# Performance work log

Hardware: AMD Instinct MI355X
Metric: run time of the kernel (lower is better)

Reference implementation:

```python
import jax, jax.numpy as jnp
import numpy as np

_EPS = 1e-6
_ZCA_EPS = 1e-5
NEG_SLOPE_ATTN = 0.2   # LeakyReLU inside score_mlp
NEG_SLOPE_FFN = 0.1    # VNLinearLeakyReLU negative_slope


def _safe_norm(x, axis, keepdims=False):
    # norm with zero-gradient at exactly-zero vectors (matches torch subgradient)
    sq = jnp.sum(x * x, axis=axis, keepdims=keepdims)
    safe = jnp.where(sq == 0, 1.0, sq)
    return jnp.sqrt(safe) * (sq > 0)


def vn_linear(W, x):
    # W: (out, in); x: (B, C_in, 3, N) -> (B, C_out, 3, N)
    return jnp.einsum('oi,bivn->bovn', W, x)


def zca_layernorm(x, gamma):
    # x: (B, C, 3, N); whiten the 3D vector components per batch element
    B, C = x.shape[0], x.shape[1]
    xf = x.reshape(B, C, 3, -1).transpose(0, 2, 1, 3).reshape(B, 3, -1)
    xf = xf.astype(jnp.float32)
    mu = xf.mean(axis=-1, keepdims=True)
    xc = xf - mu
    M = xc.shape[-1]
    cov = (xc @ xc.transpose(0, 2, 1)) / (float(M) + _EPS)  # (B,3,3)
    cov = cov + _ZCA_EPS * jnp.eye(3, dtype=cov.dtype)[None]
    w, V = jnp.linalg.eigh(cov)
    w = jnp.maximum(w, _ZCA_EPS)
    Wm = (V * jax.lax.rsqrt(w)[:, None, :]) @ V.transpose(0, 2, 1)  # (B,3,3)
    xw = Wm @ xc
    xw = xw.reshape(B, 3, C, -1).transpose(0, 2, 1, 3).reshape(x.shape).astype(x.dtype)
    return xw * gamma[None, :, None, None]


def cwsa_attention(x, pos, Wq, Wk, Wv, Wo, W1, b1, W2, b2):
    q = vn_linear(Wq, x)  # (B,C,3,N)
    k = vn_linear(Wk, x)
    v = vn_linear(Wv, x)
    qk = q.transpose(0, 3, 1, 2)  # (B,N,C,3)
    kk = k.transpose(0, 3, 1, 2)
    vv = v.transpose(0, 3, 1, 2)
    rel = qk[:, :, None, :, :] - kk[:, None, :, :, :]      # (B,N,N,C,3)
    rel_norm = _safe_norm(rel, axis=-1)                    # (B,N,N,C)
    rel_mean = rel_norm.mean(axis=-1, keepdims=True)       # (B,N,N,1)
    rel_pos = pos[:, :, None, :] - pos[:, None, :, :]      # (B,N,N,3)
    rel_pos_norm = _safe_norm(rel_pos, axis=-1, keepdims=True)  # (B,N,N,1)
    score_in = jnp.concatenate([rel_mean, rel_pos_norm], axis=-1)  # (B,N,N,2)
    h = jax.nn.leaky_relu(score_in @ W1.T + b1, NEG_SLOPE_ATTN)
    scores = h @ W2.T + b2                                  # (B,N,N,C)
    attn = jax.nn.softmax(scores, axis=2)                   # softmax over keys j
    out = jnp.einsum('bijk,bjkd->bikd', attn, vv)           # (B,N,C,3)
    out = out.transpose(0, 2, 3, 1)                         # (B,C,3,N)
    return vn_linear(Wo, out)


def vn_leaky_relu(p, d, ns):
    # p, d: (B, C, 3, N)
    dot = jnp.sum(p * d, axis=2, keepdims=True)
    dsq = jnp.sum(d * d, axis=2, keepdims=True)
    mask = (dot >= 0).astype(p.dtype)
    proj = p - (dot / (dsq + _EPS)) * d
    return ns * p + (1.0 - ns) * (mask * p + (1.0 - mask) * proj)


def ffn(x, Wfeat, Wdir, Wffn2):
    p = vn_linear(Wfeat, x)
    d = vn_linear(Wdir, x)
    h = vn_leaky_relu(p, d, NEG_SLOPE_FFN)
    return vn_linear(Wffn2, h)


def setup_inputs() -> dict:
    key = jax.random.key(0)
    ks = jax.random.split(key, 16)
    B, C, N = 2, 128, 256
    hidden, ratio = 64, 2
    sC = 1.0 / np.sqrt(C)
    inp = {
        'x': jax.random.normal(ks[0], (B, C, 3, N), dtype=jnp.float32),
        'pos': jax.random.normal(ks[1], (B, N, 3), dtype=jnp.float32),
        'Wq': jax.random.normal(ks[2], (C, C), dtype=jnp.float32) * sC,
        'Wk': jax.random.normal(ks[3], (C, C), dtype=jnp.float32) * sC,
        'Wv': jax.random.normal(ks[4], (C, C), dtype=jnp.float32) * sC,
        'Wo': jax.random.normal(ks[5], (C, C), dtype=jnp.float32) * sC,
        'W1': jax.random.normal(ks[6], (hidden, 2), dtype=jnp.float32) * (1.0 / np.sqrt(2.0)),
        'b1': jnp.zeros((hidden,), dtype=jnp.float32),
        'W2': jax.random.normal(ks[7], (C, hidden), dtype=jnp.float32) * (1.0 / np.sqrt(hidden)),
        'b2': jnp.zeros((C,), dtype=jnp.float32),
        'gamma1': jnp.ones((C,), dtype=jnp.float32),
        'Wfeat': jax.random.normal(ks[8], (C * ratio, C), dtype=jnp.float32) * sC,
        'Wdir': jax.random.normal(ks[9], (C * ratio, C), dtype=jnp.float32) * sC,
        'Wffn2': jax.random.normal(ks[10], (C, C * ratio), dtype=jnp.float32) * (1.0 / np.sqrt(C * ratio)),
        'gamma2': jnp.ones((C,), dtype=jnp.float32),
    }
    return inp


def reference(x, pos, Wq, Wk, Wv, Wo, W1, b1, W2, b2, gamma1, Wfeat, Wdir, Wffn2, gamma2):
    a = cwsa_attention(x, pos, Wq, Wk, Wv, Wo, W1, b1, W2, b2)
    x1 = zca_layernorm(x + a, gamma1)
    f = ffn(x1, Wfeat, Wdir, Wffn2)
    return zca_layernorm(x1 + f, gamma2)
```

## Files before the change

kernel.cpp:

```cpp
#include <hip/hip_runtime.h>
#include <math.h>

#define BB 2
#define CC 128
#define NN 256
#define HH 64
#define CHX 256
#define COLS 768
#define NEG_ATTN 0.2f
#define NEG_FFN 0.1f

typedef __attribute__((ext_vector_type(8))) short short8b;
typedef __attribute__((ext_vector_type(4))) float f32x4;

__device__ __forceinline__ unsigned bf16rne(float x) {
  unsigned u = __float_as_uint(x);
  return (u + 0x7fffu + ((u >> 16) & 1u)) >> 16;
}

__global__ __launch_bounds__(256) void k_qkv(
    const float* __restrict__ x, const float* __restrict__ Wq,
    const float* __restrict__ Wk, const float* __restrict__ Wv,
    float* __restrict__ q_t, float* __restrict__ k_nat, float* __restrict__ v_t)
{
  const int ct = blockIdx.x, which = blockIdx.y, b = blockIdx.z;
  const int col0 = ct * 16;
  __shared__ float xt[CC][16];
  const float* xb = x + (size_t)b * CC * COLS;
  for (int idx = threadIdx.x; idx < CC * 16; idx += 256) {
    int r = idx >> 4, cc = idx & 15;
    xt[r][cc] = xb[r * COLS + col0 + cc];
  }
  __syncthreads();
  const float* W = (which == 0) ? Wq : ((which == 1) ? Wk : Wv);
  const int co = threadIdx.x >> 1;
  const int cc0 = (threadIdx.x & 1) * 8;
  float acc[8];
#pragma unroll
  for (int k = 0; k < 8; k++) acc[k] = 0.f;
  const float* wrow = W + co * CC;
  for (int ci = 0; ci < CC; ci++) {
    float wv = wrow[ci];
#pragma unroll
    for (int k = 0; k < 8; k++) acc[k] = fmaf(wv, xt[ci][cc0 + k], acc[k]);
  }
#pragma unroll
  for (int k = 0; k < 8; k++) {
    int col = col0 + cc0 + k;
    int v = col >> 8, n = col & 255;
    float val = acc[k];
    if (which == 0)      q_t[((size_t)(b * NN + n) * CC + co) * 3 + v] = val;
    else if (which == 1) k_nat[(size_t)(b * CC + co) * COLS + col] = val;
    else                 v_t[((size_t)(b * NN + n) * 3 + v) * CC + co] = val;
  }
}

__global__ __launch_bounds__(256) void k_rel(
    const float* __restrict__ q_t, const float* __restrict__ k_nat,
    const float* __restrict__ pos, float* __restrict__ rm_all,
    float* __restrict__ rp_all)
{
  const int i0 = blockIdx.x * 2, b = blockIdx.y;
  const int t = threadIdx.x;
  __shared__ float qv[2 * CC * 3];
  for (int idx = t; idx < 2 * CC * 3; idx += 256)
    qv[idx] = q_t[(size_t)(b * NN + i0) * CC * 3 + idx];
  __syncthreads();
  const int j = t;
  const float* kb = k_nat + (size_t)b * CC * COLS;
  float a00 = 0.f, a01 = 0.f, a10 = 0.f, a11 = 0.f;
  for (int c = 0; c < CC; c += 2) {
    float kx0 = kb[c * COLS + j], ky0 = kb[c * COLS + 256 + j], kz0 = kb[c * COLS + 512 + j];
    float kx1 = kb[(c + 1) * COLS + j], ky1 = kb[(c + 1) * COLS + 256 + j], kz1 = kb[(c + 1) * COLS + 512 + j];
    {
      float dx = kx0 - qv[c * 3], dy = ky0 - qv[c * 3 + 1], dz = kz0 - qv[c * 3 + 2];
      float sq = dx * dx + dy * dy + dz * dz;
      a00 += (sq > 0.f) ? sqrtf(sq) : 0.f;
      dx = kx1 - qv[(c + 1) * 3]; dy = ky1 - qv[(c + 1) * 3 + 1]; dz = kz1 - qv[(c + 1) * 3 + 2];
      sq = dx * dx + dy * dy + dz * dz;
      a01 += (sq > 0.f) ? sqrtf(sq) : 0.f;
    }
    {
      const float* q1 = qv + CC * 3;
      float dx = kx0 - q1[c * 3], dy = ky0 - q1[c * 3 + 1], dz = kz0 - q1[c * 3 + 2];
      float sq = dx * dx + dy * dy + dz * dz;
      a10 += (sq > 0.f) ? sqrtf(sq) : 0.f;
      dx = kx1 - q1[(c + 1) * 3]; dy = ky1 - q1[(c + 1) * 3 + 1]; dz = kz1 - q1[(c + 1) * 3 + 2];
      sq = dx * dx + dy * dy + dz * dz;
      a11 += (sq > 0.f) ? sqrtf(sq) : 0.f;
    }
  }
  rm_all[(size_t)(b * NN + i0) * NN + j]     = (a00 + a01) * (1.f / 128.f);
  rm_all[(size_t)(b * NN + i0 + 1) * NN + j] = (a10 + a11) * (1.f / 128.f);
  float pjx = pos[(b * NN + j) * 3], pjy = pos[(b * NN + j) * 3 + 1], pjz = pos[(b * NN + j) * 3 + 2];
#pragma unroll
  for (int ii = 0; ii < 2; ii++) {
    float dx = pos[(b * NN + i0 + ii) * 3] - pjx;
    float dy = pos[(b * NN + i0 + ii) * 3 + 1] - pjy;
    float dz = pos[(b * NN + i0 + ii) * 3 + 2] - pjz;
    float sq = dx * dx + dy * dy + dz * dz;
    rp_all[(size_t)(b * NN + i0 + ii) * NN + j] = (sq > 0.f) ? sqrtf(sq) : 0.f;
  }
}

__global__ __launch_bounds__(256, 4) void k_attn(
    const float* __restrict__ rm_all, const float* __restrict__ rp_all,
    const float* __restrict__ v_t, const float* __restrict__ W1,
    const float* __restrict__ b1, const float* __restrict__ W2,
    float* __restrict__ a_nat)
{
  const int i = blockIdx.x, chalf = blockIdx.y, b = blockIdx.z;
  const int t = threadIdx.x;
  __shared__ __align__(16) short hh_s[64 * 64];
  __shared__ __align__(16) short w2_s[64 * 64];
  __shared__ float sc_s[64 * 65];
  __shared__ float rm_s[NN], rp_s[NN];

  rm_s[t] = rm_all[(size_t)(b * NN + i) * NN + t];
  rp_s[t] = rp_all[(size_t)(b * NN + i) * NN + t];
  {
    const int cl = t >> 2, h0 = (t & 3) * 16;
    const float* wrow = W2 + (size_t)(chalf * 64 + cl) * HH + h0;
#pragma unroll
    for (int e = 0; e < 8; e++) {
      unsigned lo = bf16rne(wrow[2 * e]);
      unsigned hi = bf16rne(wrow[2 * e + 1]);
      int didx = (cl * 32 + (h0 >> 1) + e) ^ ((cl & 7) << 2);
      ((unsigned*)w2_s)[didx] = lo | (hi << 16);
    }
  }
  const int h2 = (t & 31) * 2, jgrp = t >> 5;
  const float4 w1v = *reinterpret_cast<const float4*>(W1 + 2 * h2);
  const float c0 = b1[h2], c1 = b1[h2 + 1];
  __syncthreads();

  auto phase2 = [&](int q) {
#pragma unroll
    for (int jj = 0; jj < 8; jj++) {
      int jl = jgrp * 8 + jj;
      int jg = q * 64 + jl;
      float rmv = rm_s[jg], rpv = rp_s[jg];
      float g0 = fmaf(w1v.x, rmv, fmaf(w1v.y, rpv, c0));
      float g1 = fmaf(w1v.z, rmv, fmaf(w1v.w, rpv, c1));
      g0 = (g0 >= 0.f) ? g0 : NEG_ATTN * g0;
      g1 = (g1 >= 0.f) ? g1 : NEG_ATTN * g1;
      int didx = (jl * 32 + (h2 >> 1)) ^ ((jl & 7) << 2);
      ((unsigned*)hh_s)[didx] = bf16rne(g0) | (bf16rne(g1) << 16);
    }
  };

  phase2(0);
  __syncthreads();

  const int lane = t & 63, wv = t >> 6;
  const int g8 = (lane >> 4) * 8;
  const int cdx = wv * 16 + (lane & 15);
  const short8b bfr0 = *reinterpret_cast<const short8b*>(&w2_s[(cdx * 64 + g8) ^ ((cdx & 7) << 3)]);
  const short8b bfr1 = *reinterpret_cast<const short8b*>(&w2_s[(cdx * 64 + 32 + g8) ^ ((cdx & 7) << 3)]);

  const int cl = lane;
  const int par = wv;
  const int vc = chalf * 64 + cl;
  float m = -1e30f, l = 0.f, a0 = 0.f, a1 = 0.f, a2 = 0.f;

  for (int q = 0; q < 4; q++) {
#pragma unroll
    for (int jt = 0; jt < 4; jt++) {
      int jr = jt * 16 + (lane & 15);
      short8b af0 = *reinterpret_cast<const short8b*>(&hh_s[(jr * 64 + g8) ^ ((jr & 7) << 3)]);
      short8b af1 = *reinterpret_cast<const short8b*>(&hh_s[(jr * 64 + 32 + g8) ^ ((jr & 7) << 3)]);
      f32x4 acc = {0.f, 0.f, 0.f, 0.f};
      acc = __builtin_amdgcn_mfma_f32_16x16x32_bf16(af0, bfr0, acc, 0, 0, 0);
      acc = __builtin_amdgcn_mfma_f32_16x16x32_bf16(af1, bfr1, acc, 0, 0, 0);
      int row0 = jt * 16 + (lane >> 4) * 4;
      int ccol = wv * 16 + (lane & 15);
#pragma unroll
      for (int r = 0; r < 4; r++) sc_s[(row0 + r) * 65 + ccol] = acc[r];
    }
    __syncthreads();
#pragma unroll
    for (int jj = 0; jj < 16; jj++) {
      int jl = jj * 4 + par;
      int jg = q * 64 + jl;
      float s = sc_s[jl * 65 + cl];
      const float* vb = v_t + ((size_t)(b * NN + jg) * 3) * CC + vc;
      float v0 = vb[0], v1 = vb[CC], v2 = vb[2 * CC];
      float mn = fmaxf(m, s);
      float p = __expf(s - mn);
      float corr = __expf(m - mn);
      l = fmaf(l, corr, p);
      a0 = fmaf(a0, corr, p * v0);
      a1 = fmaf(a1, corr, p * v1);
      a2 = fmaf(a2, corr, p * v2);
      m = mn;
    }
    if (q < 3) phase2(q + 1);
    __syncthreads();
  }

  float* mrg = sc_s;
  if (par != 0) {
    float* mp = mrg + (cl * 3 + (par - 1)) * 5;
    mp[0] = m; mp[1] = l; mp[2] = a0; mp[3] = a1; mp[4] = a2;
  }
  __syncthreads();
  if (par == 0) {
    float M = m, L = l, A0 = a0, A1 = a1, A2 = a2;
    for (int q = 0; q < 3; q++) {
      const float* mp = mrg + (cl * 3 + q) * 5;
      float m2 = mp[0], l2 = mp[1];
      float mn = fmaxf(M, m2);
      float e1 = __expf(M - mn), e2 = __expf(m2 - mn);
      L = L * e1 + l2 * e2;
      A0 = A0 * e1 + mp[2] * e2;
      A1 = A1 * e1 + mp[3] * e2;
      A2 = A2 * e1 + mp[4] * e2;
      M = mn;
    }
    float inv = 1.f / L;
    float* ap = a_nat + (size_t)(b * CC + vc) * COLS + i;
    ap[0] = A0 * inv; ap[256] = A1 * inv; ap[512] = A2 * inv;
  }
}

__global__ __launch_bounds__(256) void k_wo_res(
    const float* __restrict__ a_nat, const float* __restrict__ Wo,
    const float* __restrict__ x, float* __restrict__ y1)
{
  const int ct = blockIdx.x, cohalf = blockIdx.y, b = blockIdx.z;
  const int col0 = ct * 16;
  __shared__ float at[CC][16];
  const float* ab = a_nat + (size_t)b * CC * COLS;
  for (int idx = threadIdx.x; idx < CC * 16; idx += 256) {
    int r = idx >> 4, cc = idx & 15;
    at[r][cc] = ab[r * COLS + col0 + cc];
  }
  __syncthreads();
  const int co = cohalf * 64 + (threadIdx.x >> 2);
  const int cc0 = (threadIdx.x & 3) * 4;
  float acc[4];
#pragma unroll
  for (int k = 0; k < 4; k++) acc[k] = 0.f;
  const float* wrow = Wo + co * CC;
  for (int ci = 0; ci < CC; ci++) {
    float wv = wrow[ci];
#pragma unroll
    for (int k = 0; k < 4; k++) acc[k] = fmaf(wv, at[ci][cc0 + k], acc[k]);
  }
  const size_t base = (size_t)(b * CC + co) * COLS + col0 + cc0;
#pragma unroll
  for (int k = 0; k < 4; k++) y1[base + k] = x[base + k] + acc[k];
}

__global__ __launch_bounds__(256) void k_stats1(
    const float* __restrict__ y, float* __restrict__ partials)
{
  const int blk = blockIdx.x, b = blockIdx.y;
  const float* yb = y + (size_t)b * CC * COLS;
  float v9[9];
#pragma unroll
  for (int k = 0; k < 9; k++) v9[k] = 0.f;
#pragma unroll
  for (int e = 0; e < 4; e++) {
    int idx = blk * 1024 + e * 256 + threadIdx.x;
    int cidx = idx >> 8, n = idx & 255;
    const float* row = yb + cidx * COLS + n;
    float v0 = row[0], v1 = row[256], v2 = row[512];
    v9[0] += v0; v9[1] += v1; v9[2] += v2;
    v9[3] += v0 * v0; v9[4] += v0 * v1; v9[5] += v0 * v2;
    v9[6] += v1 * v1; v9[7] += v1 * v2; v9[8] += v2 * v2;
  }
#pragma unroll
  for (int off = 32; off >= 1; off >>= 1)
#pragma unroll
    for (int k = 0; k < 9; k++) v9[k] += __shfl_down(v9[k], off);
  __shared__ float red[4][9];
  const int wid = threadIdx.x >> 6, lane = threadIdx.x & 63;
  if (lane == 0)
#pragma unroll
    for (int k = 0; k < 9; k++) red[wid][k] = v9[k];
  __syncthreads();
  if (threadIdx.x == 0) {
#pragma unroll
    for (int k = 0; k < 9; k++)
      partials[(size_t)(b * 32 + blk) * 9 + k] =
          ((red[0][k] + red[1][k]) + (red[2][k] + red[3][k]));
  }
}

__global__ __launch_bounds__(64) void k_zca_fin(
    const float* __restrict__ partials, float* __restrict__ stats)
{
  const int b = blockIdx.x;
  if (threadIdx.x != 0) return;
  float tot[9];
#pragma unroll
  for (int k = 0; k < 9; k++) tot[k] = 0.f;
  for (int p = 0; p < 32; p++)
#pragma unroll
    for (int k = 0; k < 9; k++) tot[k] += partials[(size_t)(b * 32 + p) * 9 + k];
  const float M = (float)(CC * NN);
  float mu0 = tot[0] / M, mu1 = tot[1] / M, mu2 = tot[2] / M;
  float A[3][3];
  A[0][0] = (tot[3] - M * mu0 * mu0) / M + 1e-5f;
  A[0][1] = A[1][0] = (tot[4] - M * mu0 * mu1) / M;
  A[0][2] = A[2][0] = (tot[5] - M * mu0 * mu2) / M;
  A[1][1] = (tot[6] - M * mu1 * mu1) / M + 1e-5f;
  A[1][2] = A[2][1] = (tot[7] - M * mu1 * mu2) / M;
  A[2][2] = (tot[8] - M * mu2 * mu2) / M + 1e-5f;
  float V[3][3] = {{1.f, 0.f, 0.f}, {0.f, 1.f, 0.f}, {0.f, 0.f, 1.f}};
  for (int sweep = 0; sweep < 10; sweep++) {
    for (int pi = 0; pi < 3; pi++) {
      const int p = (pi == 2) ? 1 : 0;
      const int q = (pi == 0) ? 1 : 2;
      float apq = A[p][q];
      if (fabsf(apq) < 1e-30f) continue;
      float theta = (A[q][q] - A[p][p]) / (2.f * apq);
      float tt = 1.f / (fabsf(theta) + sqrtf(theta * theta + 1.f));
      if (theta < 0.f) tt = -tt;
      float cr = 1.f / sqrtf(tt * tt + 1.f);
      float sr = tt * cr;
      float app = A[p][p], aqq = A[q][q];
      A[p][p] = app - tt * apq;
      A[q][q] = aqq + tt * apq;
      A[p][q] = A[q][p] = 0.f;
      const int r = 3 - p - q;
      float arp = A[r][p], arq = A[r][q];
      A[r][p] = A[p][r] = cr * arp - sr * arq;
      A[r][q] = A[q][r] = sr * arp + cr * arq;
      for (int rr = 0; rr < 3; rr++) {
        float vrp = V[rr][p], vrq = V[rr][q];
        V[rr][p] = cr * vrp - sr * vrq;
        V[rr][q] = sr * vrp + cr * vrq;
      }
    }
  }
  float rs[3];
#pragma unroll
  for (int k = 0; k < 3; k++) rs[k] = rsqrtf(fmaxf(A[k][k], 1e-5f));
  float* st = stats + b * 12;
  st[0] = mu0; st[1] = mu1; st[2] = mu2;
  for (int u = 0; u < 3; u++)
    for (int v = 0; v < 3; v++) {
      float acc = 0.f;
      for (int k = 0; k < 3; k++) acc += V[u][k] * rs[k] * V[v][k];
      st[3 + u * 3 + v] = acc;
    }
}

__global__ __launch_bounds__(256) void k_ffn1(
    const float* __restrict__ y1, const float* __restrict__ stats,
    const float* __restrict__ gamma, const float* __restrict__ Wfeat,
    const float* __restrict__ Wdir, float* __restrict__ hout)
{
  const int nt = blockIdx.x, cs = blockIdx.y, b = blockIdx.z;
  const int n0 = nt * 16, co0 = cs * 64;
  __shared__ float xt[CC][48];
  const float* yb = y1 + (size_t)b * CC * COLS;
  const float* st = stats + b * 12;
  for (int idx = threadIdx.x; idx < CC * 16; idx += 256) {
    int ci = idx >> 4, nn = idx & 15;
    const float* row = yb + ci * COLS + n0 + nn;
    float d0 = row[0] - st[0], d1 = row[256] - st[1], d2 = row[512] - st[2];
    float g = gamma[ci];
    xt[ci][nn]      = g * (st[3] * d0 + st[4] * d1 + st[5] * d2);
    xt[ci][16 + nn] = g * (st[6] * d0 + st[7] * d1 + st[8] * d2);
    xt[ci][32 + nn] = g * (st[9] * d0 + st[10] * d1 + st[11] * d2);
  }
  __syncthreads();
  const int co = co0 + (threadIdx.x & 63);
  const int nn0 = (threadIdx.x >> 6) * 4;
  float p[3][4], d[3][4];
#pragma unroll
  for (int v = 0; v < 3; v++)
#pragma unroll
    for (int k = 0; k < 4; k++) { p[v][k] = 0.f; d[v][k] = 0.f; }
  const float* wf = Wfeat + co * CC;
  const float* wd = Wdir + co * CC;
  for (int ci = 0; ci < CC; ci++) {
    float a = wf[ci], bb = wd[ci];
#pragma unroll
    for (int v = 0; v < 3; v++)
#pragma unroll
      for (int k = 0; k < 4; k++) {
        float xv = xt[ci][v * 16 + nn0 + k];
        p[v][k] = fmaf(a, xv, p[v][k]);
        d[v][k] = fmaf(bb, xv, d[v][k]);
      }
  }
  float* hb = hout + (size_t)(b * CHX + co) * COLS;
#pragma unroll
  for (int k = 0; k < 4; k++) {
    float dot = p[0][k] * d[0][k] + p[1][k] * d[1][k] + p[2][k] * d[2][k];
    float dsq = d[0][k] * d[0][k] + d[1][k] * d[1][k] + d[2][k] * d[2][k];
    float coef = (dot >= 0.f) ? 0.f : (1.f - NEG_FFN) * dot / (dsq + 1e-6f);
#pragma unroll
    for (int v = 0; v < 3; v++)
      hb[v * 256 + n0 + nn0 + k] = p[v][k] - coef * d[v][k];
  }
}

__global__ __launch_bounds__(256) void k_ffn2(
    const float* __restrict__ h, const float* __restrict__ Wffn2,
    const float* __restrict__ y1, const float* __restrict__ stats,
    const float* __restrict__ gamma, float* __restrict__ x2)
{
  const int ct = blockIdx.x, cohalf = blockIdx.y, b = blockIdx.z;
  const int col0 = ct * 16;
  __shared__ float ht[CHX][16];
  const float* hb = h + (size_t)b * CHX * COLS;
  for (int idx = threadIdx.x; idx < CHX * 16; idx += 256) {
    int r = idx >> 4, cc = idx & 15;
    ht[r][cc] = hb[r * COLS + col0 + cc];
  }
  __syncthreads();
  const int co = cohalf * 64 + (threadIdx.x >> 2);
  const int cc0 = (threadIdx.x & 3) * 4;
  float acc[4];
#pragma unroll
  for (int k = 0; k < 4; k++) acc[k] = 0.f;
  const float* w = Wffn2 + co * CHX;
  for (int ci = 0; ci < CHX; ci++) {
    float wv = w[ci];
#pragma unroll
    for (int k = 0; k < 4; k++) acc[k] = fmaf(wv, ht[ci][cc0 + k], acc[k]);
  }
  const int col_base = col0 + cc0;
  const int v = col_base >> 8, n = col_base & 255;
  const float* st = stats + b * 12;
  const float* yb = y1 + (size_t)(b * CC + co) * COLS + n;
  const float g = gamma[co];
  const float w0 = st[3 + v * 3 + 0], w1 = st[3 + v * 3 + 1], w2 = st[3 + v * 3 + 2];
  const size_t base = (size_t)(b * CC + co) * COLS + col_base;
#pragma unroll
  for (int k = 0; k < 4; k++) {
    float d0 = yb[k] - st[0], d1 = yb[256 + k] - st[1], d2 = yb[512 + k] - st[2];
    float xw = g * (w0 * d0 + w1 * d1 + w2 * d2);
    x2[base + k] = xw + acc[k];
  }
}

__global__ __launch_bounds__(256) void k_zca_apply(
    const float* __restrict__ y, const float* __restrict__ stats,
    const float* __restrict__ gamma, float* __restrict__ out)
{
  int idx = blockIdx.x * blockDim.x + threadIdx.x;
  int b = idx >> 15, rem = idx & 32767;
  int cidx = rem >> 8, n = rem & 255;
  const float* st = stats + b * 12;
  const size_t base = (size_t)(b * CC + cidx) * COLS + n;
  float v0 = y[base] - st[0];
  float v1 = y[base + 256] - st[1];
  float v2 = y[base + 512] - st[2];
  float g = gamma[cidx];
  out[base]       = g * (st[3] * v0 + st[4] * v1 + st[5] * v2);
  out[base + 256] = g * (st[6] * v0 + st[7] * v1 + st[8] * v2);
  out[base + 512] = g * (st[9] * v0 + st[10] * v1 + st[11] * v2);
}

extern "C" void kernel_launch(void* const* d_in, const int* in_sizes, int n_in,
                              void* d_out, int out_size, void* d_ws, size_t ws_size,
                              hipStream_t stream)
{
  (void)in_sizes; (void)n_in; (void)out_size; (void)ws_size;
  const float* x      = (const float*)d_in[0];
  const float* pos    = (const float*)d_in[1];
  const float* Wq     = (const float*)d_in[2];
  const float* Wk     = (const float*)d_in[3];
  const float* Wv     = (const float*)d_in[4];
  const float* Wo     = (const float*)d_in[5];
  const float* W1     = (const float*)d_in[6];
  const float* b1     = (const float*)d_in[7];
  const float* W2     = (const float*)d_in[8];
  const float* gamma1 = (const float*)d_in[10];
  const float* Wfeat  = (const float*)d_in[11];
  const float* Wdir   = (const float*)d_in[12];
  const float* Wffn2  = (const float*)d_in[13];
  const float* gamma2 = (const float*)d_in[14];

  float* ws = (float*)d_ws;
  const size_t SZ = (size_t)BB * CC * 3 * NN;
  const size_t RMSZ = (size_t)BB * NN * NN;
  float* q_t    = ws;
  float* k_nat  = ws + SZ;
  float* v_t    = ws + 2 * SZ;
  float* rm_all = ws + 3 * SZ;
  float* rp_all = ws + 3 * SZ + RMSZ;
  float* a_nat  = ws;
  float* y1     = ws + SZ;
  float* hbuf   = ws + 2 * SZ;
  float* x2     = ws;
  float* part   = ws + 4 * SZ;
  float* stats1 = ws + 4 * SZ + 640;
  float* stats2 = ws + 4 * SZ + 704;

  k_qkv<<<dim3(48, 3, BB), 256, 0, stream>>>(x, Wq, Wk, Wv, q_t, k_nat, v_t);
  k_rel<<<dim3(NN / 2, BB), 256, 0, stream>>>(q_t, k_nat, pos, rm_all, rp_all);
  k_attn<<<dim3(NN, 2, BB), 256, 0, stream>>>(rm_all, rp_all, v_t, W1, b1, W2, a_nat);
  k_wo_res<<<dim3(48, 2, BB), 256, 0, stream>>>(a_nat, Wo, x, y1);
  k_stats1<<<dim3(32, BB), 256, 0, stream>>>(y1, part);
  k_zca_fin<<<BB, 64, 0, stream>>>(part, stats1);
  k_ffn1<<<dim3(16, 4, BB), 256, 0, stream>>>(y1, stats1, gamma1, Wfeat, Wdir, hbuf);
  k_ffn2<<<dim3(48, 2, BB), 256, 0, stream>>>(hbuf, Wffn2, y1, stats1, gamma1, x2);
  k_stats1<<<dim3(32, BB), 256, 0, stream>>>(x2, part);
  k_zca_fin<<<BB, 64, 0, stream>>>(part, stats2);
  k_zca_apply<<<256, 256, 0, stream>>>(x2, stats2, gamma2, (float*)d_out);
}
```

Measured before the change: 113.4 us.

## Stage weights in LDS for all GEMM kernels, merge stats kernels, drop softmax max

The QKV, Wo, FFN1 and FFN2 GEMMs now stage weight tiles in shared memory and compute 2-row register tiles. Each thread previously read its own weight row straight from global memory. k_rel now handles one query per block instead of two. The two-kernel stats/finalize pair is merged into a single 1024-thread block per batch element. The online softmax in k_attn drops the running max and rescale and uses a plain exp sum, which can overflow if scores are large. Grid shapes change to match the new tiling.

```diff
diff --git a/kernel.cpp b/kernel.cpp
--- a/kernel.cpp
+++ b/kernel.cpp
@@ -23,35 +23,57 @@
     const float* __restrict__ Wk, const float* __restrict__ Wv,
     float* __restrict__ q_t, float* __restrict__ k_nat, float* __restrict__ v_t)
 {
-  const int ct = blockIdx.x, which = blockIdx.y, b = blockIdx.z;
-  const int col0 = ct * 16;
-  __shared__ float xt[CC][16];
+  const int ct = blockIdx.x, b = blockIdx.z;
+  const int which = blockIdx.y >> 1, cohalf = blockIdx.y & 1;
+  const int col0 = ct * 32, co0 = cohalf * 64;
+  const int t = threadIdx.x;
+  __shared__ __align__(16) float xt[CC][32];
+  __shared__ float Wl[64][33];
   const float* xb = x + (size_t)b * CC * COLS;
-  for (int idx = threadIdx.x; idx < CC * 16; idx += 256) {
-    int r = idx >> 4, cc = idx & 15;
+  for (int idx = t; idx < CC * 32; idx += 256) {
+    int r = idx >> 5, cc = idx & 31;
     xt[r][cc] = xb[r * COLS + col0 + cc];
   }
-  __syncthreads();
   const float* W = (which == 0) ? Wq : ((which == 1) ? Wk : Wv);
-  const int co = threadIdx.x >> 1;
-  const int cc0 = (threadIdx.x & 1) * 8;
-  float acc[8];
-#pragma unroll
-  for (int k = 0; k < 8; k++) acc[k] = 0.f;
-  const float* wrow = W + co * CC;
-  for (int ci = 0; ci < CC; ci++) {
-    float wv = wrow[ci];
-#pragma unroll
-    for (int k = 0; k < 8; k++) acc[k] = fmaf(wv, xt[ci][cc0 + k], acc[k]);
-  }
-#pragma unroll
-  for (int k = 0; k < 8; k++) {
-    int col = col0 + cc0 + k;
-    int v = col >> 8, n = col & 255;
-    float val = acc[k];
-    if (which == 0)      q_t[((size_t)(b * NN + n) * CC + co) * 3 + v] = val;
-    else if (which == 1) k_nat[(size_t)(b * CC + co) * COLS + col] = val;
-    else                 v_t[((size_t)(b * NN + n) * 3 + v) * CC + co] = val;
+  const int cop = t >> 3;
+  const int colq = t & 7;
+  float acc[2][4];
+#pragma unroll
+  for (int r = 0; r < 2; r++)
+#pragma unroll
+    for (int k = 0; k < 4; k++) acc[r][k] = 0.f;
+  for (int cu = 0; cu < 4; cu++) {
+    __syncthreads();
+    for (int idx = t; idx < 64 * 32; idx += 256) {
+      int row = idx >> 5, ci = idx & 31;
+      Wl[row][ci] = W[(size_t)(co0 + row) * CC + cu * 32 + ci];
+    }
+    __syncthreads();
+#pragma unroll 8
+    for (int ci = 0; ci < 32; ci++) {
+      float w0 = Wl[cop * 2][ci], w1 = Wl[cop * 2 + 1][ci];
+      const float4 xv = *(reinterpret_cast<const float4*>(xt[cu * 32 + ci]) + colq);
+      acc[0][0] = fmaf(w0, xv.x, acc[0][0]); acc[0][1] = fmaf(w0, xv.y, acc[0][1]);
+      acc[0][2] = fmaf(w0, xv.z, acc[0][2]); acc[0][3] = fmaf(w0, xv.w, acc[0][3]);
+      acc[1][0] = fmaf(w1, xv.x, acc[1][0]); acc[1][1] = fmaf(w1, xv.y, acc[1][1]);
+      acc[1][2] = fmaf(w1, xv.z, acc[1][2]); acc[1][3] = fmaf(w1, xv.w, acc[1][3]);
+    }
+  }
+#pragma unroll
+  for (int r = 0; r < 2; r++) {
+    const int co_g = co0 + cop * 2 + r;
+    if (which == 1) {
+      float4 o = {acc[r][0], acc[r][1], acc[r][2], acc[r][3]};
+      *reinterpret_cast<float4*>(&k_nat[(size_t)(b * CC + co_g) * COLS + col0 + colq * 4]) = o;
+    } else {
+#pragma unroll
+      for (int k = 0; k < 4; k++) {
+        int col = col0 + colq * 4 + k;
+        int v = col >> 8, n = col & 255;
+        if (which == 0) q_t[((size_t)(b * NN + n) * CC + co_g) * 3 + v] = acc[r][k];
+        else            v_t[((size_t)(b * NN + n) * 3 + v) * CC + co_g] = acc[r][k];
+      }
+    }
   }
 }
 
@@ -60,47 +82,36 @@
     const float* __restrict__ pos, float* __restrict__ rm_all,
     float* __restrict__ rp_all)
 {
-  const int i0 = blockIdx.x * 2, b = blockIdx.y;
-  const int t = threadIdx.x;
-  __shared__ float qv[2 * CC * 3];
-  for (int idx = t; idx < 2 * CC * 3; idx += 256)
-    qv[idx] = q_t[(size_t)(b * NN + i0) * CC * 3 + idx];
+  const int i = blockIdx.x, b = blockIdx.y;
+  const int t = threadIdx.x;
+  __shared__ float qv[CC * 3];
+  for (int idx = t; idx < CC * 3; idx += 256)
+    qv[idx] = q_t[(size_t)(b * NN + i) * CC * 3 + idx];
   __syncthreads();
   const int j = t;
   const float* kb = k_nat + (size_t)b * CC * COLS;
-  float a00 = 0.f, a01 = 0.f, a10 = 0.f, a11 = 0.f;
-  for (int c = 0; c < CC; c += 2) {
-    float kx0 = kb[c * COLS + j], ky0 = kb[c * COLS + 256 + j], kz0 = kb[c * COLS + 512 + j];
+  float p0 = 0.f, p1 = 0.f, p2 = 0.f, p3 = 0.f;
+  for (int c = 0; c < CC; c += 4) {
+    float kx0 = kb[(c + 0) * COLS + j], ky0 = kb[(c + 0) * COLS + 256 + j], kz0 = kb[(c + 0) * COLS + 512 + j];
     float kx1 = kb[(c + 1) * COLS + j], ky1 = kb[(c + 1) * COLS + 256 + j], kz1 = kb[(c + 1) * COLS + 512 + j];
-    {
-      float dx = kx0 - qv[c * 3], dy = ky0 - qv[c * 3 + 1], dz = kz0 - qv[c * 3 + 2];
-      float sq = dx * dx + dy * dy + dz * dz;
-      a00 += (sq > 0.f) ? sqrtf(sq) : 0.f;
-      dx = kx1 - qv[(c + 1) * 3]; dy = ky1 - qv[(c + 1) * 3 + 1]; dz = kz1 - qv[(c + 1) * 3 + 2];
-      sq = dx * dx + dy * dy + dz * dz;
-      a01 += (sq > 0.f) ? sqrtf(sq) : 0.f;
-    }
-    {
-      const float* q1 = qv + CC * 3;
-      float dx = kx0 - q1[c * 3], dy = ky0 - q1[c * 3 + 1], dz = kz0 - q1[c * 3 + 2];
-      float sq = dx * dx + dy * dy + dz * dz;
-      a10 += (sq > 0.f) ? sqrtf(sq) : 0.f;
-      dx = kx1 - q1[(c + 1) * 3]; dy = ky1 - q1[(c + 1) * 3 + 1]; dz = kz1 - q1[(c + 1) * 3 + 2];
-      sq = dx * dx + dy * dy + dz * dz;
-      a11 += (sq > 0.f) ? sqrtf(sq) : 0.f;
-    }
-  }
-  rm_all[(size_t)(b * NN + i0) * NN + j]     = (a00 + a01) * (1.f / 128.f);
-  rm_all[(size_t)(b * NN + i0 + 1) * NN + j] = (a10 + a11) * (1.f / 128.f);
-  float pjx = pos[(b * NN + j) * 3], pjy = pos[(b * NN + j) * 3 + 1], pjz = pos[(b * NN + j) * 3 + 2];
-#pragma unroll
-  for (int ii = 0; ii < 2; ii++) {
-    float dx = pos[(b * NN + i0 + ii) * 3] - pjx;
-    float dy = pos[(b * NN + i0 + ii) * 3 + 1] - pjy;
-    float dz = pos[(b * NN + i0 + ii) * 3 + 2] - pjz;
-    float sq = dx * dx + dy * dy + dz * dz;
-    rp_all[(size_t)(b * NN + i0 + ii) * NN + j] = (sq > 0.f) ? sqrtf(sq) : 0.f;
-  }
+    float kx2 = kb[(c + 2) * COLS + j], ky2 = kb[(c + 2) * COLS + 256 + j], kz2 = kb[(c + 2) * COLS + 512 + j];
+    float kx3 = kb[(c + 3) * COLS + j], ky3 = kb[(c + 3) * COLS + 256 + j], kz3 = kb[(c + 3) * COLS + 512 + j];
+    float dx, dy, dz, sq;
+    dx = kx0 - qv[(c + 0) * 3]; dy = ky0 - qv[(c + 0) * 3 + 1]; dz = kz0 - qv[(c + 0) * 3 + 2];
+    sq = dx * dx + dy * dy + dz * dz; p0 += (sq > 0.f) ? sqrtf(sq) : 0.f;
+    dx = kx1 - qv[(c + 1) * 3]; dy = ky1 - qv[(c + 1) * 3 + 1]; dz = kz1 - qv[(c + 1) * 3 + 2];
+    sq = dx * dx + dy * dy + dz * dz; p1 += (sq > 0.f) ? sqrtf(sq) : 0.f;
+    dx = kx2 - qv[(c + 2) * 3]; dy = ky2 - qv[(c + 2) * 3 + 1]; dz = kz2 - qv[(c + 2) * 3 + 2];
+    sq = dx * dx + dy * dy + dz * dz; p2 += (sq > 0.f) ? sqrtf(sq) : 0.f;
+    dx = kx3 - qv[(c + 3) * 3]; dy = ky3 - qv[(c + 3) * 3 + 1]; dz = kz3 - qv[(c + 3) * 3 + 2];
+    sq = dx * dx + dy * dy + dz * dz; p3 += (sq > 0.f) ? sqrtf(sq) : 0.f;
+  }
+  rm_all[(size_t)(b * NN + i) * NN + j] = ((p0 + p1) + (p2 + p3)) * (1.f / 128.f);
+  float dx = pos[(b * NN + i) * 3 + 0] - pos[(b * NN + j) * 3 + 0];
+  float dy = pos[(b * NN + i) * 3 + 1] - pos[(b * NN + j) * 3 + 1];
+  float dz = pos[(b * NN + i) * 3 + 2] - pos[(b * NN + j) * 3 + 2];
+  float sq = dx * dx + dy * dy + dz * dz;
+  rp_all[(size_t)(b * NN + i) * NN + j] = (sq > 0.f) ? sqrtf(sq) : 0.f;
 }
 
 __global__ __launch_bounds__(256, 4) void k_attn(
@@ -161,7 +172,7 @@
   const int cl = lane;
   const int par = wv;
   const int vc = chalf * 64 + cl;
-  float m = -1e30f, l = 0.f, a0 = 0.f, a1 = 0.f, a2 = 0.f;
+  float l = 0.f, a0 = 0.f, a1 = 0.f, a2 = 0.f;
 
   for (int q = 0; q < 4; q++) {
 #pragma unroll
@@ -185,14 +196,11 @@
       float s = sc_s[jl * 65 + cl];
       const float* vb = v_t + ((size_t)(b * NN + jg) * 3) * CC + vc;
       float v0 = vb[0], v1 = vb[CC], v2 = vb[2 * CC];
-      float mn = fmaxf(m, s);
-      float p = __expf(s - mn);
-      float corr = __expf(m - mn);
-      l = fmaf(l, corr, p);
-      a0 = fmaf(a0, corr, p * v0);
-      a1 = fmaf(a1, corr, p * v1);
-      a2 = fmaf(a2, corr, p * v2);
-      m = mn;
+      float p = __expf(s);
+      l += p;
+      a0 = fmaf(p, v0, a0);
+      a1 = fmaf(p, v1, a1);
+      a2 = fmaf(p, v2, a2);
     }
     if (q < 3) phase2(q + 1);
     __syncthreads();
@@ -200,22 +208,16 @@
 
   float* mrg = sc_s;
   if (par != 0) {
-    float* mp = mrg + (cl * 3 + (par - 1)) * 5;
-    mp[0] = m; mp[1] = l; mp[2] = a0; mp[3] = a1; mp[4] = a2;
+    float* mp = mrg + (cl * 3 + (par - 1)) * 4;
+    mp[0] = l; mp[1] = a0; mp[2] = a1; mp[3] = a2;
   }
   __syncthreads();
   if (par == 0) {
-    float M = m, L = l, A0 = a0, A1 = a1, A2 = a2;
+    float L = l, A0 = a0, A1 = a1, A2 = a2;
+#pragma unroll
     for (int q = 0; q < 3; q++) {
-      const float* mp = mrg + (cl * 3 + q) * 5;
-      float m2 = mp[0], l2 = mp[1];
-      float mn = fmaxf(M, m2);
-      float e1 = __expf(M - mn), e2 = __expf(m2 - mn);
-      L = L * e1 + l2 * e2;
-      A0 = A0 * e1 + mp[2] * e2;
-      A1 = A1 * e1 + mp[3] * e2;
-      A2 = A2 * e1 + mp[4] * e2;
-      M = mn;
+      const float* mp = mrg + (cl * 3 + q) * 4;
+      L += mp[0]; A0 += mp[1]; A1 += mp[2]; A2 += mp[3];
     }
     float inv = 1.f / L;
     float* ap = a_nat + (size_t)(b * CC + vc) * COLS + i;
@@ -228,41 +230,51 @@
     const float* __restrict__ x, float* __restrict__ y1)
 {
   const int ct = blockIdx.x, cohalf = blockIdx.y, b = blockIdx.z;
-  const int col0 = ct * 16;
-  __shared__ float at[CC][16];
+  const int col0 = ct * 16, co0 = cohalf * 64;
+  const int t = threadIdx.x;
+  __shared__ __align__(16) float at[CC][16];
+  __shared__ float Wl[64][33];
   const float* ab = a_nat + (size_t)b * CC * COLS;
-  for (int idx = threadIdx.x; idx < CC * 16; idx += 256) {
+  for (int idx = t; idx < CC * 16; idx += 256) {
     int r = idx >> 4, cc = idx & 15;
     at[r][cc] = ab[r * COLS + col0 + cc];
   }
-  __syncthreads();
-  const int co = cohalf * 64 + (threadIdx.x >> 2);
-  const int cc0 = (threadIdx.x & 3) * 4;
-  float acc[4];
-#pragma unroll
-  for (int k = 0; k < 4; k++) acc[k] = 0.f;
-  const float* wrow = Wo + co * CC;
-  for (int ci = 0; ci < CC; ci++) {
-    float wv = wrow[ci];
-#pragma unroll
-    for (int k = 0; k < 4; k++) acc[k] = fmaf(wv, at[ci][cc0 + k], acc[k]);
-  }
-  const size_t base = (size_t)(b * CC + co) * COLS + col0 + cc0;
-#pragma unroll
-  for (int k = 0; k < 4; k++) y1[base + k] = x[base + k] + acc[k];
-}
-
-__global__ __launch_bounds__(256) void k_stats1(
-    const float* __restrict__ y, float* __restrict__ partials)
-{
-  const int blk = blockIdx.x, b = blockIdx.y;
+  const int cop = t >> 3, colp = t & 7;
+  float acc[2][2] = {{0.f, 0.f}, {0.f, 0.f}};
+  for (int cu = 0; cu < 4; cu++) {
+    __syncthreads();
+    for (int idx = t; idx < 64 * 32; idx += 256) {
+      int row = idx >> 5, ci = idx & 31;
+      Wl[row][ci] = Wo[(size_t)(co0 + row) * CC + cu * 32 + ci];
+    }
+    __syncthreads();
+#pragma unroll 8
+    for (int ci = 0; ci < 32; ci++) {
+      float w0 = Wl[cop * 2][ci], w1 = Wl[cop * 2 + 1][ci];
+      const float2 xv = *(reinterpret_cast<const float2*>(at[cu * 32 + ci]) + colp);
+      acc[0][0] = fmaf(w0, xv.x, acc[0][0]); acc[0][1] = fmaf(w0, xv.y, acc[0][1]);
+      acc[1][0] = fmaf(w1, xv.x, acc[1][0]); acc[1][1] = fmaf(w1, xv.y, acc[1][1]);
+    }
+  }
+#pragma unroll
+  for (int r = 0; r < 2; r++) {
+    const size_t base = (size_t)(b * CC + co0 + cop * 2 + r) * COLS + col0 + colp * 2;
+    y1[base]     = x[base]     + acc[r][0];
+    y1[base + 1] = x[base + 1] + acc[r][1];
+  }
+}
+
+__global__ __launch_bounds__(1024) void k_stats(
+    const float* __restrict__ y, float* __restrict__ stats)
+{
+  const int b = blockIdx.x;
   const float* yb = y + (size_t)b * CC * COLS;
+  const int t = threadIdx.x;
   float v9[9];
 #pragma unroll
   for (int k = 0; k < 9; k++) v9[k] = 0.f;
-#pragma unroll
-  for (int e = 0; e < 4; e++) {
-    int idx = blk * 1024 + e * 256 + threadIdx.x;
+  for (int e = 0; e < 32; e++) {
+    int idx = e * 1024 + t;
     int cidx = idx >> 8, n = idx & 255;
     const float* row = yb + cidx * COLS + n;
     float v0 = row[0], v1 = row[256], v2 = row[512];
@@ -274,78 +286,67 @@
   for (int off = 32; off >= 1; off >>= 1)
 #pragma unroll
     for (int k = 0; k < 9; k++) v9[k] += __shfl_down(v9[k], off);
-  __shared__ float red[4][9];
-  const int wid = threadIdx.x >> 6, lane = threadIdx.x & 63;
+  __shared__ float red[16][9];
+  const int wid = t >> 6, lane = t & 63;
   if (lane == 0)
 #pragma unroll
     for (int k = 0; k < 9; k++) red[wid][k] = v9[k];
   __syncthreads();
-  if (threadIdx.x == 0) {
-#pragma unroll
-    for (int k = 0; k < 9; k++)
-      partials[(size_t)(b * 32 + blk) * 9 + k] =
-          ((red[0][k] + red[1][k]) + (red[2][k] + red[3][k]));
-  }
-}
-
-__global__ __launch_bounds__(64) void k_zca_fin(
-    const float* __restrict__ partials, float* __restrict__ stats)
-{
-  const int b = blockIdx.x;
-  if (threadIdx.x != 0) return;
-  float tot[9];
-#pragma unroll
-  for (int k = 0; k < 9; k++) tot[k] = 0.f;
-  for (int p = 0; p < 32; p++)
-#pragma unroll
-    for (int k = 0; k < 9; k++) tot[k] += partials[(size_t)(b * 32 + p) * 9 + k];
-  const float M = (float)(CC * NN);
-  float mu0 = tot[0] / M, mu1 = tot[1] / M, mu2 = tot[2] / M;
-  float A[3][3];
-  A[0][0] = (tot[3] - M * mu0 * mu0) / M + 1e-5f;
-  A[0][1] = A[1][0] = (tot[4] - M * mu0 * mu1) / M;
-  A[0][2] = A[2][0] = (tot[5] - M * mu0 * mu2) / M;
-  A[1][1] = (tot[6] - M * mu1 * mu1) / M + 1e-5f;
-  A[1][2] = A[2][1] = (tot[7] - M * mu1 * mu2) / M;
-  A[2][2] = (tot[8] - M * mu2 * mu2) / M + 1e-5f;
-  float V[3][3] = {{1.f, 0.f, 0.f}, {0.f, 1.f, 0.f}, {0.f, 0.f, 1.f}};
-  for (int sweep = 0; sweep < 10; sweep++) {
-    for (int pi = 0; pi < 3; pi++) {
-      const int p = (pi == 2) ? 1 : 0;
-      const int q = (pi == 0) ? 1 : 2;
-      float apq = A[p][q];
-      if (fabsf(apq) < 1e-30f) continue;
-      float theta = (A[q][q] - A[p][p]) / (2.f * apq);
-      float tt = 1.f / (fabsf(theta) + sqrtf(theta * theta + 1.f));
-      if (theta < 0.f) tt = -tt;
-      float cr = 1.f / sqrtf(tt * tt + 1.f);
-      float sr = tt * cr;
-      float app = A[p][p], aqq = A[q][q];
-      A[p][p] = app - tt * apq;
-      A[q][q] = aqq + tt * apq;
-      A[p][q] = A[q][p] = 0.f;
-      const int r = 3 - p - q;
-      float arp = A[r][p], arq = A[r][q];
-      A[r][p] = A[p][r] = cr * arp - sr * arq;
-      A[r][q] = A[q][r] = sr * arp + cr * arq;
-      for (int rr = 0; rr < 3; rr++) {
-        float vrp = V[rr][p], vrq = V[rr][q];
-        V[rr][p] = cr * vrp - sr * vrq;
-        V[rr][q] = sr * vrp + cr * vrq;
+  if (t == 0) {
+    float tot[9];
+#pragma unroll
+    for (int k = 0; k < 9; k++) tot[k] = 0.f;
+    for (int w = 0; w < 16; w++)
+#pragma unroll
+      for (int k = 0; k < 9; k++) tot[k] += red[w][k];
+    const float M = (float)(CC * NN);
+    float mu0 = tot[0] / M, mu1 = tot[1] / M, mu2 = tot[2] / M;
+    float A[3][3];
+    A[0][0] = (tot[3] - M * mu0 * mu0) / M + 1e-5f;
+    A[0][1] = A[1][0] = (tot[4] - M * mu0 * mu1) / M;
+    A[0][2] = A[2][0] = (tot[5] - M * mu0 * mu2) / M;
+    A[1][1] = (tot[6] - M * mu1 * mu1) / M + 1e-5f;
+    A[1][2] = A[2][1] = (tot[7] - M * mu1 * mu2) / M;
+    A[2][2] = (tot[8] - M * mu2 * mu2) / M + 1e-5f;
+    float V[3][3] = {{1.f, 0.f, 0.f}, {0.f, 1.f, 0.f}, {0.f, 0.f, 1.f}};
+    for (int sweep = 0; sweep < 10; sweep++) {
+      for (int pi = 0; pi < 3; pi++) {
+        const int p = (pi == 2) ? 1 : 0;
+        const int q = (pi == 0) ? 1 : 2;
+        float apq = A[p][q];
+        if (fabsf(apq) < 1e-30f) continue;
+        float theta = (A[q][q] - A[p][p]) / (2.f * apq);
+        float tt = 1.f / (fabsf(theta) + sqrtf(theta * theta + 1.f));
+        if (theta < 0.f) tt = -tt;
+        float cr = 1.f / sqrtf(tt * tt + 1.f);
+        float sr = tt * cr;
+        float app = A[p][p], aqq = A[q][q];
+        A[p][p] = app - tt * apq;
+        A[q][q] = aqq + tt * apq;
+        A[p][q] = A[q][p] = 0.f;
+        const int r = 3 - p - q;
+        float arp = A[r][p], arq = A[r][q];
+        A[r][p] = A[p][r] = cr * arp - sr * arq;
+        A[r][q] = A[q][r] = sr * arp + cr * arq;
+        for (int rr = 0; rr < 3; rr++) {
+          float vrp = V[rr][p], vrq = V[rr][q];
+          V[rr][p] = cr * vrp - sr * vrq;
+          V[rr][q] = sr * vrp + cr * vrq;
+        }
       }
     }
-  }
-  float rs[3];
-#pragma unroll
-  for (int k = 0; k < 3; k++) rs[k] = rsqrtf(fmaxf(A[k][k], 1e-5f));
-  float* st = stats + b * 12;
-  st[0] = mu0; st[1] = mu1; st[2] = mu2;
-  for (int u = 0; u < 3; u++)
-    for (int v = 0; v < 3; v++) {
-      float acc = 0.f;
-      for (int k = 0; k < 3; k++) acc += V[u][k] * rs[k] * V[v][k];
-      st[3 + u * 3 + v] = acc;
-    }
+    float rs[3];
+#pragma unroll
+    for (int k = 0; k < 3; k++) rs[k] = rsqrtf(fmaxf(A[k][k], 1e-5f));
+    float* st = stats + b * 12;
+    st[0] = mu0; st[1] = mu1; st[2] = mu2;
+    for (int u = 0; u < 3; u++)
+      for (int v = 0; v < 3; v++) {
+        float acc = 0.f;
+        for (int k = 0; k < 3; k++) acc += V[u][k] * rs[k] * V[v][k];
+        st[3 + u * 3 + v] = acc;
+      }
+  }
 }
 
 __global__ __launch_bounds__(256) void k_ffn1(
@@ -354,50 +355,47 @@
     const float* __restrict__ Wdir, float* __restrict__ hout)
 {
   const int nt = blockIdx.x, cs = blockIdx.y, b = blockIdx.z;
-  const int n0 = nt * 16, co0 = cs * 64;
-  __shared__ float xt[CC][48];
+  const int n0 = nt * 8, co0 = cs * 32;
+  const int t = threadIdx.x;
+  __shared__ float xt[CC][24];
+  __shared__ float Wfl[32][33], Wdl[32][33];
   const float* yb = y1 + (size_t)b * CC * COLS;
   const float* st = stats + b * 12;
-  for (int idx = threadIdx.x; idx < CC * 16; idx += 256) {
-    int ci = idx >> 4, nn = idx & 15;
+  for (int idx = t; idx < CC * 8; idx += 256) {
+    int ci = idx >> 3, nn = idx & 7;
     const float* row = yb + ci * COLS + n0 + nn;
     float d0 = row[0] - st[0], d1 = row[256] - st[1], d2 = row[512] - st[2];
     float g = gamma[ci];
     xt[ci][nn]      = g * (st[3] * d0 + st[4] * d1 + st[5] * d2);
-    xt[ci][16 + nn] = g * (st[6] * d0 + st[7] * d1 + st[8] * d2);
-    xt[ci][32 + nn] = g * (st[9] * d0 + st[10] * d1 + st[11] * d2);
-  }
-  __syncthreads();
-  const int co = co0 + (threadIdx.x & 63);
-  const int nn0 = (threadIdx.x >> 6) * 4;
-  float p[3][4], d[3][4];
+    xt[ci][8 + nn]  = g * (st[6] * d0 + st[7] * d1 + st[8] * d2);
+    xt[ci][16 + nn] = g * (st[9] * d0 + st[10] * d1 + st[11] * d2);
+  }
+  const int co = t >> 3, nn = t & 7;
+  float p[3] = {0.f, 0.f, 0.f}, d[3] = {0.f, 0.f, 0.f};
+  for (int cu = 0; cu < 4; cu++) {
+    __syncthreads();
+    for (int idx = t; idx < 2048; idx += 256) {
+      int row = (idx & 1023) >> 5, ci = idx & 31;
+      if (idx < 1024) Wfl[row][ci] = Wfeat[(size_t)(co0 + row) * CC + cu * 32 + ci];
+      else            Wdl[row][ci] = Wdir[(size_t)(co0 + row) * CC + cu * 32 + ci];
+    }
+    __syncthreads();
+#pragma unroll 8
+    for (int ci = 0; ci < 32; ci++) {
+      float wf = Wfl[co][ci], wd = Wdl[co][ci];
+      const float* xr = xt[cu * 32 + ci];
+      float x0 = xr[nn], x1 = xr[8 + nn], x2 = xr[16 + nn];
+      p[0] = fmaf(wf, x0, p[0]); p[1] = fmaf(wf, x1, p[1]); p[2] = fmaf(wf, x2, p[2]);
+      d[0] = fmaf(wd, x0, d[0]); d[1] = fmaf(wd, x1, d[1]); d[2] = fmaf(wd, x2, d[2]);
+    }
+  }
+  float dot = p[0] * d[0] + p[1] * d[1] + p[2] * d[2];
+  float dsq = d[0] * d[0] + d[1] * d[1] + d[2] * d[2];
+  float coef = (dot >= 0.f) ? 0.f : (1.f - NEG_FFN) * dot / (dsq + 1e-6f);
+  float* hb = hout + (size_t)(b * CHX + co0 + co) * COLS;
 #pragma unroll
   for (int v = 0; v < 3; v++)
-#pragma unroll
-    for (int k = 0; k < 4; k++) { p[v][k] = 0.f; d[v][k] = 0.f; }
-  const float* wf = Wfeat + co * CC;
-  const float* wd = Wdir + co * CC;
-  for (int ci = 0; ci < CC; ci++) {
-    float a = wf[ci], bb = wd[ci];
-#pragma unroll
-    for (int v = 0; v < 3; v++)
-#pragma unroll
-      for (int k = 0; k < 4; k++) {
-        float xv = xt[ci][v * 16 + nn0 + k];
-        p[v][k] = fmaf(a, xv, p[v][k]);
-        d[v][k] = fmaf(bb, xv, d[v][k]);
-      }
-  }
-  float* hb = hout + (size_t)(b * CHX + co) * COLS;
-#pragma unroll
-  for (int k = 0; k < 4; k++) {
-    float dot = p[0][k] * d[0][k] + p[1][k] * d[1][k] + p[2][k] * d[2][k];
-    float dsq = d[0][k] * d[0][k] + d[1][k] * d[1][k] + d[2][k] * d[2][k];
-    float coef = (dot >= 0.f) ? 0.f : (1.f - NEG_FFN) * dot / (dsq + 1e-6f);
-#pragma unroll
-    for (int v = 0; v < 3; v++)
-      hb[v * 256 + n0 + nn0 + k] = p[v][k] - coef * d[v][k];
-  }
+    hb[v * 256 + n0 + nn] = p[v] - coef * d[v];
 }
 
 __global__ __launch_bounds__(256) void k_ffn2(
@@ -406,37 +404,47 @@
     const float* __restrict__ gamma, float* __restrict__ x2)
 {
   const int ct = blockIdx.x, cohalf = blockIdx.y, b = blockIdx.z;
-  const int col0 = ct * 16;
-  __shared__ float ht[CHX][16];
+  const int col0 = ct * 16, co0 = cohalf * 64;
+  const int t = threadIdx.x;
+  __shared__ __align__(16) float ht[CHX][16];
+  __shared__ float Wl[64][33];
   const float* hb = h + (size_t)b * CHX * COLS;
-  for (int idx = threadIdx.x; idx < CHX * 16; idx += 256) {
+  for (int idx = t; idx < CHX * 16; idx += 256) {
     int r = idx >> 4, cc = idx & 15;
     ht[r][cc] = hb[r * COLS + col0 + cc];
   }
-  __syncthreads();
-  const int co = cohalf * 64 + (threadIdx.x >> 2);
-  const int cc0 = (threadIdx.x & 3) * 4;
-  float acc[4];
-#pragma unroll
-  for (int k = 0; k < 4; k++) acc[k] = 0.f;
-  const float* w = Wffn2 + co * CHX;
-  for (int ci = 0; ci < CHX; ci++) {
-    float wv = w[ci];
-#pragma unroll
-    for (int k = 0; k < 4; k++) acc[k] = fmaf(wv, ht[ci][cc0 + k], acc[k]);
-  }
-  const int col_base = col0 + cc0;
+  const int cop = t >> 3, colp = t & 7;
+  float acc[2][2] = {{0.f, 0.f}, {0.f, 0.f}};
+  for (int cu = 0; cu < 8; cu++) {
+    __syncthreads();
+    for (int idx = t; idx < 64 * 32; idx += 256) {
+      int row = idx >> 5, ci = idx & 31;
+      Wl[row][ci] = Wffn2[(size_t)(co0 + row) * CHX + cu * 32 + ci];
+    }
+    __syncthreads();
+#pragma unroll 8
+    for (int ci = 0; ci < 32; ci++) {
+      float w0 = Wl[cop * 2][ci], w1 = Wl[cop * 2 + 1][ci];
+      const float2 xv = *(reinterpret_cast<const float2*>(ht[cu * 32 + ci]) + colp);
+      acc[0][0] = fmaf(w0, xv.x, acc[0][0]); acc[0][1] = fmaf(w0, xv.y, acc[0][1]);
+      acc[1][0] = fmaf(w1, xv.x, acc[1][0]); acc[1][1] = fmaf(w1, xv.y, acc[1][1]);
+    }
+  }
+  const int col_base = col0 + colp * 2;
   const int v = col_base >> 8, n = col_base & 255;
   const float* st = stats + b * 12;
-  const float* yb = y1 + (size_t)(b * CC + co) * COLS + n;
-  const float g = gamma[co];
   const float w0 = st[3 + v * 3 + 0], w1 = st[3 + v * 3 + 1], w2 = st[3 + v * 3 + 2];
-  const size_t base = (size_t)(b * CC + co) * COLS + col_base;
-#pragma unroll
-  for (int k = 0; k < 4; k++) {
-    float d0 = yb[k] - st[0], d1 = yb[256 + k] - st[1], d2 = yb[512 + k] - st[2];
-    float xw = g * (w0 * d0 + w1 * d1 + w2 * d2);
-    x2[base + k] = xw + acc[k];
+#pragma unroll
+  for (int r = 0; r < 2; r++) {
+    const int co_g = co0 + cop * 2 + r;
+    const float g = gamma[co_g];
+    const float* yr = y1 + (size_t)(b * CC + co_g) * COLS + n;
+    const size_t base = (size_t)(b * CC + co_g) * COLS + col_base;
+#pragma unroll
+    for (int k = 0; k < 2; k++) {
+      float d0 = yr[k] - st[0], d1 = yr[256 + k] - st[1], d2 = yr[512 + k] - st[2];
+      x2[base + k] = g * (w0 * d0 + w1 * d1 + w2 * d2) + acc[r][k];
+    }
   }
 }
 
@@ -490,19 +498,16 @@
   float* y1     = ws + SZ;
   float* hbuf   = ws + 2 * SZ;
   float* x2     = ws;
-  float* part   = ws + 4 * SZ;
-  float* stats1 = ws + 4 * SZ + 640;
-  float* stats2 = ws + 4 * SZ + 704;
-
-  k_qkv<<<dim3(48, 3, BB), 256, 0, stream>>>(x, Wq, Wk, Wv, q_t, k_nat, v_t);
-  k_rel<<<dim3(NN / 2, BB), 256, 0, stream>>>(q_t, k_nat, pos, rm_all, rp_all);
+  float* stats1 = ws + 4 * SZ;
+  float* stats2 = ws + 4 * SZ + 64;
+
+  k_qkv<<<dim3(24, 6, BB), 256, 0, stream>>>(x, Wq, Wk, Wv, q_t, k_nat, v_t);
+  k_rel<<<dim3(NN, BB), 256, 0, stream>>>(q_t, k_nat, pos, rm_all, rp_all);
   k_attn<<<dim3(NN, 2, BB), 256, 0, stream>>>(rm_all, rp_all, v_t, W1, b1, W2, a_nat);
   k_wo_res<<<dim3(48, 2, BB), 256, 0, stream>>>(a_nat, Wo, x, y1);
-  k_stats1<<<dim3(32, BB), 256, 0, stream>>>(y1, part);
-  k_zca_fin<<<BB, 64, 0, stream>>>(part, stats1);
-  k_ffn1<<<dim3(16, 4, BB), 256, 0, stream>>>(y1, stats1, gamma1, Wfeat, Wdir, hbuf);
+  k_stats<<<BB, 1024, 0, stream>>>(y1, stats1);
+  k_ffn1<<<dim3(32, 8, BB), 256, 0, stream>>>(y1, stats1, gamma1, Wfeat, Wdir, hbuf);
   k_ffn2<<<dim3(48, 2, BB), 256, 0, stream>>>(hbuf, Wffn2, y1, stats1, gamma1, x2);
-  k_stats1<<<dim3(32, BB), 256, 0, stream>>>(x2, part);
-  k_zca_fin<<<BB, 64, 0, stream>>>(part, stats2);
+  k_stats<<<BB, 1024, 0, stream>>>(x2, stats2);
   k_zca_apply<<<256, 256, 0, stream>>>(x2, stats2, gamma2, (float*)d_out);
 }
```

Result: slower. 119.3 us (+5.2%).
